# Kernel optimization log

Measured on AMD Instinct MI355X. Metric: run time of the kernel, lower is better.

## Reference

```python
import jax, jax.numpy as jnp
import numpy as np


def setup_inputs() -> dict:
    key = jax.random.key(0)
    ks = jax.random.split(key, 8)
    B, C, H, W = 4, 256, 64, 64
    s = 1.0 / np.sqrt(C)
    return {
        "x": jax.random.normal(ks[0], (B, C, H, W), jnp.float32),
        "y": jax.random.normal(ks[1], (B, C, H, W), jnp.float32),
        "Wq": jax.random.normal(ks[2], (C, C), jnp.float32) * s,
        "bq": jax.random.normal(ks[3], (C,), jnp.float32) * 0.01,
        "Wk": jax.random.normal(ks[4], (C, C), jnp.float32) * s,
        "bk": jax.random.normal(ks[5], (C,), jnp.float32) * 0.01,
        "Wv": jax.random.normal(ks[6], (C, C), jnp.float32) * s,
        "bv": jax.random.normal(ks[7], (C,), jnp.float32) * 0.01,
    }


def reference(x, y, Wq, bq, Wk, bk, Wv, bv):
    B, C, H, W = x.shape
    N = H * W
    # 1x1 convs == per-pixel linear over channels. Flatten spatial to N.
    xf = x.reshape(B, C, N)  # [B,C,N]
    yf = y.reshape(B, C, N)
    # q: [B,N,C]; k: [B,C,N]; v: [B,N,C]
    q = jnp.einsum('oc,bcn->bno', Wq, xf) + bq[None, None, :]
    k = jnp.einsum('oc,bcn->bon', Wk, yf) + bk[None, :, None]
    v = jnp.einsum('oc,bcn->bno', Wv, yf) + bv[None, None, :]
    # attention scores [B,N,N]; NOTE: original has no 1/sqrt(d) scaling.
    attn = jax.nn.softmax(jnp.einsum('bnc,bcm->bnm', q, k), axis=-1)
    out = jnp.einsum('bnm,bmc->bnc', attn, v)  # [B,N,C]
    return out.transpose(0, 2, 1).reshape(B, C, H, W)
```

## Files before the change

kernel.cpp:

```cpp
#include <hip/hip_runtime.h>


typedef __attribute__((ext_vector_type(8))) short short8;
typedef __attribute__((ext_vector_type(4))) float f32x4;
typedef __attribute__((ext_vector_type(4))) int int4v;
typedef __attribute__((ext_vector_type(8))) _Float16 half8;

#define LOG2E 1.44269504089f

static __device__ __forceinline__ float exp2_fast(float x){ return __builtin_amdgcn_exp2f(x); }

static __device__ __forceinline__ int pk_f16(float a, float b){
  auto h = __builtin_amdgcn_cvt_pkrtz(a, b);
  return __builtin_bit_cast(int, h);
}
static __device__ __forceinline__ unsigned short f2h(float v){
  return __builtin_bit_cast(unsigned short, (_Float16)v);
}

#define GLOAD16(gp, lp) __builtin_amdgcn_global_load_lds( \
  (const __attribute__((address_space(1))) void*)(gp),    \
  (__attribute__((address_space(3))) void*)(lp), 16, 0, 0)

#define MFMAF16(a,b,c) __builtin_amdgcn_mfma_f32_16x16x32_f16( \
  __builtin_bit_cast(half8, a), __builtin_bit_cast(half8, b), c, 0, 0, 0)

__global__ __launch_bounds__(256) void cvt_w(
    const float* __restrict__ wq, const float* __restrict__ wk,
    const float* __restrict__ wv, unsigned short* __restrict__ wf)
{
  const int o = blockIdx.x, t = blockIdx.y, c = threadIdx.x;
  const float* w = (t == 0) ? wq : ((t == 1) ? wk : wv);
  wf[t*65536 + o*256 + c] = f2h(w[o*256 + c]);
}

__global__ __launch_bounds__(256, 2) void proj_kernel(
    const float* __restrict__ x, const float* __restrict__ y,
    const unsigned short* __restrict__ wf,
    const float* __restrict__ bq, const float* __restrict__ bk, const float* __restrict__ bv,
    unsigned short* __restrict__ qf, unsigned short* __restrict__ kf,
    unsigned short* __restrict__ vtf)
{
  __shared__ float xs[256*64];
  __shared__ short wlds[2][4096];

  const int t   = blockIdx.z;
  const int b   = blockIdx.y;
  const int n0  = blockIdx.x * 64;
  const int tid = threadIdx.x;
  const int w   = tid >> 6, lane = tid & 63, g = lane >> 4, l15 = lane & 15;

  const float* src = ((t == 0) ? x : y) + (size_t)b*1048576 + n0;
  const char*  wt_b = (const char*)(wf + t*65536);

  int wsrc[2];
  #pragma unroll
  for (int i = 0; i < 2; i++){
    int s = w*2 + i;
    int row = s*2 + (lane >> 5);
    wsrc[i] = row*512 + (((lane & 31)*16) ^ ((row & 7) << 4));
  }

  #pragma unroll
  for (int i = 0; i < 16; i++){
    int c  = i*16 + (tid >> 4);
    int gg = (c >> 3) & 3;
    int sg = ((tid & 15) - 4*gg) & 15;
    GLOAD16((const char*)src + (size_t)c*16384 + sg*16,
            (char*)xs + (i*256 + tid)*16);
  }
  #pragma unroll
  for (int i = 0; i < 2; i++){
    int s = w*2 + i;
    GLOAD16(wt_b + wsrc[i], (char*)&wlds[0][0] + s*1024);
  }
  __syncthreads();

  int4v xf[8];
  {
    const int nn = (w*16 + l15 + 16*g) & 63;
    #pragma unroll
    for (int cs = 0; cs < 8; cs++){
      float v[8];
      #pragma unroll
      for (int j = 0; j < 8; j++) v[j] = xs[(cs*32 + g*8 + j)*64 + nn];
      int4v f;
      f[0] = pk_f16(v[0], v[1]); f[1] = pk_f16(v[2], v[3]);
      f[2] = pk_f16(v[4], v[5]); f[3] = pk_f16(v[6], v[7]);
      xf[cs] = f;
    }
  }

  const float* bias = (t == 0) ? bq : ((t == 1) ? bk : bv);

  int buf = 0;
  for (int ot = 0; ot < 16; ot++){
    if (ot < 15){
      #pragma unroll
      for (int i = 0; i < 2; i++){
        int s = w*2 + i;
        GLOAD16(wt_b + (ot+1)*8192 + wsrc[i], (char*)&wlds[buf^1][0] + s*1024);
      }
    }

    f32x4 acc;
    if (t < 2){
      float bo = bias[ot*16 + l15];
      acc = (f32x4){bo, bo, bo, bo};
    } else {
      acc = *(const f32x4*)&bias[ot*16 + g*4];
    }
    const char* wb = (const char*)&wlds[buf][0];
    #pragma unroll
    for (int cs = 0; cs < 8; cs++){
      short8 wfr = *(const short8*)(wb + (l15*512 + ((cs*64 + g*16) ^ ((l15 & 7) << 4))));
      if (t < 2) acc = MFMAF16(__builtin_bit_cast(short8, xf[cs]), wfr, acc);
      else       acc = MFMAF16(wfr, __builtin_bit_cast(short8, xf[cs]), acc);
    }
    if (t < 2){
      unsigned short* outp = (t == 0) ? qf : kf;
      #pragma unroll
      for (int r = 0; r < 4; r++){
        int n = n0 + w*16 + g*4 + r;
        outp[((size_t)(b*4096 + n))*256 + ot*16 + l15] = f2h(acc[r]);
      }
    } else {
      #pragma unroll
      for (int r = 0; r < 4; r++){
        int o = ot*16 + g*4 + r;
        vtf[((size_t)(b*256 + o))*4096 + n0 + w*16 + l15] = f2h(acc[r]);
      }
    }
    __syncthreads();
    buf ^= 1;
  }
}

__global__ __launch_bounds__(512, 2) void attn_kernel(
    const unsigned short* __restrict__ qf, const unsigned short* __restrict__ kf,
    const unsigned short* __restrict__ vtf,
    float* __restrict__ outp, unsigned short* __restrict__ part,
    float* __restrict__ mlbuf, int nsplit, int iters)
{
  __shared__ short k_s[3*32*256];
  __shared__ short v_s[3*256*32];

  const int tid  = threadIdx.x;
  const int w    = tid >> 6, lane = tid & 63, g = lane >> 4, col = lane & 15;
  const int bid  = blockIdx.x;

  int b, kvq, qt;
  if (nsplit == 4){
    int xcd = bid & 7, s = bid >> 3;
    int combo = xcd*2 + (s >> 4);
    qt = s & 15;  b = combo >> 2;  kvq = combo & 3;
  } else {
    int combo = bid & 7;
    qt = bid >> 3;  b = combo >> 1;  kvq = combo & 1;
  }
  const int qbase = qt * 256;

  short8 qh[2][8];
  #pragma unroll
  for (int nn = 0; nn < 2; nn++){
    const size_t qoff = ((size_t)(b*4096 + qbase + w*32 + nn*16 + col))*256 + g*8;
    #pragma unroll
    for (int ch = 0; ch < 8; ch++)
      qh[nn][ch] = *(const short8*)(qf + qoff + ch*32);
  }

  f32x4 o_acc[2][16];
  #pragma unroll
  for (int nn = 0; nn < 2; nn++)
    #pragma unroll
    for (int i = 0; i < 16; i++){
      o_acc[nn][i][0]=0.f; o_acc[nn][i][1]=0.f; o_acc[nn][i][2]=0.f; o_acc[nn][i][3]=0.f;
    }
  float mst[2] = {-1e30f, -1e30f};
  float lst[2] = {0.f, 0.f};

  const int swzK = (col & 7) << 4;
  const int g16  = g << 4;
  const int kb0  = col * 512;
  const int kb1  = kb0 + 8192;
  const int vb   = col*64 + (g16 ^ (((col>>1)&3)<<4));

  const int laneA  = col + ((g & 1) ? 32 : 0);
  const int laneB  = laneA + 16;
  const bool selLow = (g < 2);

  int ksrc[2], vsrc[2];
  #pragma unroll
  for (int i = 0; i < 2; i++){
    int s = w*2 + i;
    int m = s*2 + (lane >> 5);
    ksrc[i] = m*512 + (((lane & 31)*16) ^ ((m & 7) << 4));
    int c = s*16 + (lane >> 2);
    vsrc[i] = c*8192 + (((lane & 3)*16) ^ (((lane >> 3) & 3) << 4));
  }

  const int rows = 4096 / nsplit;
  const char* khg = (const char*)(kf + ((size_t)b*4096 + kvq*rows)*256);
  const char* vg  = (const char*)(vtf + ((size_t)b*256)*4096) + kvq*rows*2;

  #pragma unroll
  for (int i = 0; i < 2; i++){
    int s = w*2 + i;
    GLOAD16(khg + ksrc[i], (char*)k_s + s*1024);
    GLOAD16(vg  + vsrc[i], (char*)v_s + s*1024);
  }

  int cur = 0, nxt = 1;
  for (int it = 0; it < iters; ++it){
    if (it + 1 < iters){
      const char* kht = khg + (size_t)(it+1)*16384;
      const char* vtt = vg  + (size_t)(it+1)*64;
      const int ko = nxt*16384, vo = nxt*16384;
      #pragma unroll
      for (int i = 0; i < 2; i++){
        int s = w*2 + i;
        GLOAD16(kht + ksrc[i], (char*)k_s + ko + s*1024);
        GLOAD16(vtt + vsrc[i], (char*)v_s + vo + s*1024);
      }
      asm volatile("s_waitcnt vmcnt(4)" ::: "memory");
    } else {
      asm volatile("s_waitcnt vmcnt(0)" ::: "memory");
    }
    __builtin_amdgcn_s_barrier();
    __builtin_amdgcn_sched_barrier(0);

    const char* kb   = (const char*)k_s + cur*16384;
    const char* vbuf = (const char*)v_s + cur*16384;

    f32x4 s00 = {0.f,0.f,0.f,0.f}, s01 = {0.f,0.f,0.f,0.f};
    f32x4 s10 = {0.f,0.f,0.f,0.f}, s11 = {0.f,0.f,0.f,0.f};
    __builtin_amdgcn_s_setprio(1);
    #pragma unroll
    for (int ch = 0; ch < 8; ch++){
      int inr = ((ch << 6) | g16) ^ swzK;
      short8 kh0 = *(const short8*)(kb + kb0 + inr);
      short8 kh1 = *(const short8*)(kb + kb1 + inr);
      s00 = MFMAF16(kh0, qh[0][ch], s00);
      s01 = MFMAF16(kh1, qh[0][ch], s01);
      s10 = MFMAF16(kh0, qh[1][ch], s10);
      s11 = MFMAF16(kh1, qh[1][ch], s11);
    }
    __builtin_amdgcn_s_setprio(0);

    short8 pf[2];
    #pragma unroll
    for (int nn = 0; nn < 2; nn++){
      f32x4 s0 = nn ? s10 : s00;
      f32x4 s1 = nn ? s11 : s01;
      float tmax = fmaxf(fmaxf(fmaxf(s0[0],s0[1]), fmaxf(s0[2],s0[3])),
                         fmaxf(fmaxf(s1[0],s1[1]), fmaxf(s1[2],s1[3])));
      tmax = fmaxf(tmax, __shfl_xor(tmax, 16));
      tmax = fmaxf(tmax, __shfl_xor(tmax, 32));

      if (__any(tmax > mst[nn])){
        float mn = fmaxf(mst[nn], tmax);
        float sc = exp2_fast((mst[nn] - mn) * LOG2E);
        lst[nn] *= sc;
        #pragma unroll
        for (int i = 0; i < 16; i++){
          o_acc[nn][i][0]*=sc; o_acc[nn][i][1]*=sc;
          o_acc[nn][i][2]*=sc; o_acc[nn][i][3]*=sc;
        }
        mst[nn] = mn;
      }
      const float mb = mst[nn] * LOG2E;
      float p0 = exp2_fast(s0[0]*LOG2E - mb);
      float p1 = exp2_fast(s0[1]*LOG2E - mb);
      float p2 = exp2_fast(s0[2]*LOG2E - mb);
      float p3 = exp2_fast(s0[3]*LOG2E - mb);
      float p4 = exp2_fast(s1[0]*LOG2E - mb);
      float p5 = exp2_fast(s1[1]*LOG2E - mb);
      float p6 = exp2_fast(s1[2]*LOG2E - mb);
      float p7 = exp2_fast(s1[3]*LOG2E - mb);

      float psum = ((p0+p1)+(p2+p3)) + ((p4+p5)+(p6+p7));
      psum += __shfl_xor(psum, 16);
      psum += __shfl_xor(psum, 32);
      lst[nn] += psum;

      int W0 = pk_f16(p0, p1);
      int W1 = pk_f16(p2, p3);
      int W2 = pk_f16(p4, p5);
      int W3 = pk_f16(p6, p7);

      int a0 = __shfl(W0, laneA), a1 = __shfl(W1, laneA);
      int a2 = __shfl(W2, laneA), a3 = __shfl(W3, laneA);
      int b0 = __shfl(W0, laneB), b1 = __shfl(W1, laneB);
      int b2 = __shfl(W2, laneB), b3 = __shfl(W3, laneB);
      int4v ti;
      ti[0] = selLow ? a0 : a2;
      ti[1] = selLow ? a1 : a3;
      ti[2] = selLow ? b0 : b2;
      ti[3] = selLow ? b1 : b3;
      pf[nn] = __builtin_bit_cast(short8, ti);
    }

    __builtin_amdgcn_s_setprio(1);
    #pragma unroll
    for (int ct = 0; ct < 16; ct++){
      short8 vf = *(const short8*)(vbuf + ct*1024 + vb);
      o_acc[0][ct] = MFMAF16(vf, pf[0], o_acc[0][ct]);
      o_acc[1][ct] = MFMAF16(vf, pf[1], o_acc[1][ct]);
    }
    __builtin_amdgcn_s_setprio(0);

    cur = nxt;
    nxt = (nxt + 1 == 3) ? 0 : nxt + 1;
  }

  #pragma unroll
  for (int nn = 0; nn < 2; nn++){
    const int n = qbase + w*32 + nn*16 + col;
    if (kvq == 0){
      #pragma unroll
      for (int ct = 0; ct < 16; ct++)
        #pragma unroll
        for (int r = 0; r < 4; r++){
          int c = ct*16 + g*4 + r;
          outp[((size_t)(b*256 + c))*4096 + n] = o_acc[nn][ct][r];
        }
    } else {
      const size_t pbase = ((size_t)((kvq-1)*1024 + b*256))*4096;
      #pragma unroll
      for (int ct = 0; ct < 16; ct++)
        #pragma unroll
        for (int r = 0; r < 4; r++){
          int c = ct*16 + g*4 + r;
          part[pbase + (size_t)c*4096 + n] = f2h(o_acc[nn][ct][r]);
        }
    }
    if (g == 0){
      const size_t mb2 = ((size_t)(kvq*4 + b)*4096 + n)*2;
      mlbuf[mb2]     = mst[nn];
      mlbuf[mb2 + 1] = lst[nn];
    }
  }
}

__global__ __launch_bounds__(256) void merge_kernel(
    const unsigned short* __restrict__ part, const float* __restrict__ mlbuf,
    float* __restrict__ out, int nsplit)
{
  const int T    = blockIdx.x*256 + threadIdx.x;
  const int rowc = T >> 9;
  const int n8   = (T & 511) * 8;
  const int b    = rowc >> 8;

  float num[8], den[8], m[8];
  {
    f32x4 a0 = *(const f32x4*)&out[(size_t)rowc*4096 + n8];
    f32x4 a1 = *(const f32x4*)&out[(size_t)rowc*4096 + n8 + 4];
    const float* mlp = &mlbuf[((size_t)b*4096 + n8)*2];
    #pragma unroll
    for (int j = 0; j < 8; j++){
      m[j]   = mlp[j*2];
      den[j] = mlp[j*2 + 1];
      num[j] = (j < 4) ? a0[j] : a1[j-4];
    }
  }
  for (int s = 1; s < nsplit; s++){
    short8 pv = *(const short8*)&part[((size_t)((s-1)*1024 + rowc))*4096 + n8];
    const float* mlp = &mlbuf[((size_t)(s*4 + b)*4096 + n8)*2];
    #pragma unroll
    for (int j = 0; j < 8; j++){
      float ms = mlp[j*2], ls = mlp[j*2 + 1];
      unsigned short u = (unsigned short)pv[j];
      float ps = (float)*(const _Float16*)&u;
      float mn = fmaxf(m[j], ms);
      float sa = exp2_fast((m[j] - mn) * LOG2E);
      float sb = exp2_fast((ms   - mn) * LOG2E);
      num[j] = num[j]*sa + ps*sb;
      den[j] = den[j]*sa + ls*sb;
      m[j] = mn;
    }
  }
  f32x4 o0, o1;
  #pragma unroll
  for (int j = 0; j < 8; j++){
    float v = num[j] / den[j];
    if (j < 4) o0[j] = v; else o1[j-4] = v;
  }
  float* op = out + (size_t)rowc*4096 + n8;
  *(f32x4*)op       = o0;
  *(f32x4*)(op + 4) = o1;
}

extern "C" void kernel_launch(void* const* d_in, const int* in_sizes, int n_in,
                              void* d_out, int out_size, void* d_ws, size_t ws_size,
                              hipStream_t stream)
{
  const float* x  = (const float*)d_in[0];
  const float* y  = (const float*)d_in[1];
  const float* Wq = (const float*)d_in[2];
  const float* bq = (const float*)d_in[3];
  const float* Wk = (const float*)d_in[4];
  const float* bk = (const float*)d_in[5];
  const float* Wv = (const float*)d_in[6];
  const float* bv = (const float*)d_in[7];
  float* out = (float*)d_out;

  char* ws = (char*)d_ws;
  const size_t MB = 1048576;
  unsigned short* qf   = (unsigned short*)(ws + 0*MB);
  unsigned short* kfp  = (unsigned short*)(ws + 8*MB);
  unsigned short* vtf  = (unsigned short*)(ws + 16*MB);
  unsigned short* wf   = (unsigned short*)(ws + 24*MB);
  unsigned short* part = (unsigned short*)(ws + 24*MB + 393216);

  const int nsplit = (ws_size >= 50*MB) ? 4 : 2;
  const int iters  = (4096 / nsplit) / 32;
  float* mlb = (float*)(ws + 24*MB + 393216 + (size_t)(nsplit-1)*8*MB);

  cvt_w<<<dim3(256,3), dim3(256), 0, stream>>>(Wq, Wk, Wv, wf);
  proj_kernel<<<dim3(64,4,3), dim3(256), 0, stream>>>(x, y, wf, bq, bk, bv,
                                                      qf, kfp, vtf);
  attn_kernel<<<dim3(64*nsplit), dim3(512), 0, stream>>>(qf, kfp, vtf, out, part,
                                                         mlb, nsplit, iters);
  merge_kernel<<<dim3(2048), dim3(256), 0, stream>>>(part, mlb, out, nsplit);
}
```

Before: 159.7 us.

## Software-pipeline QK^T one tile ahead with 4-stage LDS ring buffer

Restructures the attention loop so the QK^T MFMAs for tile it+1 are issued before the softmax and PV work of tile it. K/V prefetch now runs two tiles ahead using a 4-deep LDS ring instead of a 3-deep one. The aim is to overlap matrix-core work with the exp/shuffle softmax phase and hide more global-load latency. The cost is more LDS (256KB of staging per 2 blocks may limit occupancy or fail launch_bounds(512,2)) and more live accumulator registers.

```diff
diff --git a/kernel.cpp b/kernel.cpp
--- a/kernel.cpp
+++ b/kernel.cpp
@@ -142,8 +142,8 @@
     float* __restrict__ outp, unsigned short* __restrict__ part,
     float* __restrict__ mlbuf, int nsplit, int iters)
 {
-  __shared__ short k_s[3*32*256];
-  __shared__ short v_s[3*256*32];
+  __shared__ short k_s[4*32*256];
+  __shared__ short v_s[4*256*32];
 
   const int tid  = threadIdx.x;
   const int w    = tid >> 6, lane = tid & 63, g = lane >> 4, col = lane & 15;
@@ -203,55 +203,79 @@
   const char* khg = (const char*)(kf + ((size_t)b*4096 + kvq*rows)*256);
   const char* vg  = (const char*)(vtf + ((size_t)b*256)*4096) + kvq*rows*2;
 
-  #pragma unroll
-  for (int i = 0; i < 2; i++){
-    int s = w*2 + i;
-    GLOAD16(khg + ksrc[i], (char*)k_s + s*1024);
-    GLOAD16(vg  + vsrc[i], (char*)v_s + s*1024);
-  }
-
-  int cur = 0, nxt = 1;
-  for (int it = 0; it < iters; ++it){
-    if (it + 1 < iters){
-      const char* kht = khg + (size_t)(it+1)*16384;
-      const char* vtt = vg  + (size_t)(it+1)*64;
-      const int ko = nxt*16384, vo = nxt*16384;
-      #pragma unroll
-      for (int i = 0; i < 2; i++){
-        int s = w*2 + i;
-        GLOAD16(kht + ksrc[i], (char*)k_s + ko + s*1024);
-        GLOAD16(vtt + vsrc[i], (char*)v_s + vo + s*1024);
-      }
-      asm volatile("s_waitcnt vmcnt(4)" ::: "memory");
-    } else {
-      asm volatile("s_waitcnt vmcnt(0)" ::: "memory");
-    }
-    __builtin_amdgcn_s_barrier();
-    __builtin_amdgcn_sched_barrier(0);
-
-    const char* kb   = (const char*)k_s + cur*16384;
-    const char* vbuf = (const char*)v_s + cur*16384;
-
-    f32x4 s00 = {0.f,0.f,0.f,0.f}, s01 = {0.f,0.f,0.f,0.f};
-    f32x4 s10 = {0.f,0.f,0.f,0.f}, s11 = {0.f,0.f,0.f,0.f};
+#define STAGE_TILE(T, BSEL) do {                                   \
+    const char* kht_ = khg + (size_t)(T)*16384;                    \
+    const char* vtt_ = vg  + (size_t)(T)*64;                       \
+    const int off_ = (BSEL)*16384;                                 \
+    _Pragma("unroll")                                              \
+    for (int i_ = 0; i_ < 2; i_++){                                \
+      int s_ = w*2 + i_;                                           \
+      GLOAD16(kht_ + ksrc[i_], (char*)k_s + off_ + s_*1024);       \
+      GLOAD16(vtt_ + vsrc[i_], (char*)v_s + off_ + s_*1024);       \
+    }                                                              \
+  } while (0)
+
+  STAGE_TILE(0, 0);
+  STAGE_TILE(1, 1);
+  asm volatile("s_waitcnt vmcnt(4)" ::: "memory");
+  __builtin_amdgcn_s_barrier();
+  __builtin_amdgcn_sched_barrier(0);
+
+  f32x4 n00 = {0.f,0.f,0.f,0.f}, n01 = {0.f,0.f,0.f,0.f};
+  f32x4 n10 = {0.f,0.f,0.f,0.f}, n11 = {0.f,0.f,0.f,0.f};
+  {
+    const char* kb = (const char*)k_s;
     __builtin_amdgcn_s_setprio(1);
     #pragma unroll
     for (int ch = 0; ch < 8; ch++){
       int inr = ((ch << 6) | g16) ^ swzK;
       short8 kh0 = *(const short8*)(kb + kb0 + inr);
       short8 kh1 = *(const short8*)(kb + kb1 + inr);
-      s00 = MFMAF16(kh0, qh[0][ch], s00);
-      s01 = MFMAF16(kh1, qh[0][ch], s01);
-      s10 = MFMAF16(kh0, qh[1][ch], s10);
-      s11 = MFMAF16(kh1, qh[1][ch], s11);
+      n00 = MFMAF16(kh0, qh[0][ch], n00);
+      n01 = MFMAF16(kh1, qh[0][ch], n01);
+      n10 = MFMAF16(kh0, qh[1][ch], n10);
+      n11 = MFMAF16(kh1, qh[1][ch], n11);
     }
     __builtin_amdgcn_s_setprio(0);
+  }
+
+  for (int it = 0; it < iters; ++it){
+    if (it + 2 < iters){
+      STAGE_TILE(it + 2, (it + 2) & 3);
+      asm volatile("s_waitcnt vmcnt(4)" ::: "memory");
+    } else {
+      asm volatile("s_waitcnt vmcnt(0)" ::: "memory");
+    }
+    if (it + 1 < iters){
+      __builtin_amdgcn_s_barrier();
+      __builtin_amdgcn_sched_barrier(0);
+    }
+
+    f32x4 c00 = n00, c01 = n01, c10 = n10, c11 = n11;
+
+    if (it + 1 < iters){
+      const char* kb = (const char*)k_s + ((it + 1) & 3)*16384;
+      n00 = (f32x4){0.f,0.f,0.f,0.f}; n01 = (f32x4){0.f,0.f,0.f,0.f};
+      n10 = (f32x4){0.f,0.f,0.f,0.f}; n11 = (f32x4){0.f,0.f,0.f,0.f};
+      __builtin_amdgcn_s_setprio(1);
+      #pragma unroll
+      for (int ch = 0; ch < 8; ch++){
+        int inr = ((ch << 6) | g16) ^ swzK;
+        short8 kh0 = *(const short8*)(kb + kb0 + inr);
+        short8 kh1 = *(const short8*)(kb + kb1 + inr);
+        n00 = MFMAF16(kh0, qh[0][ch], n00);
+        n01 = MFMAF16(kh1, qh[0][ch], n01);
+        n10 = MFMAF16(kh0, qh[1][ch], n10);
+        n11 = MFMAF16(kh1, qh[1][ch], n11);
+      }
+      __builtin_amdgcn_s_setprio(0);
+    }
 
     short8 pf[2];
     #pragma unroll
     for (int nn = 0; nn < 2; nn++){
-      f32x4 s0 = nn ? s10 : s00;
-      f32x4 s1 = nn ? s11 : s01;
+      f32x4 s0 = nn ? c10 : c00;
+      f32x4 s1 = nn ? c11 : c01;
       float tmax = fmaxf(fmaxf(fmaxf(s0[0],s0[1]), fmaxf(s0[2],s0[3])),
                          fmaxf(fmaxf(s1[0],s1[1]), fmaxf(s1[2],s1[3])));
       tmax = fmaxf(tmax, __shfl_xor(tmax, 16));
@@ -300,6 +324,7 @@
       pf[nn] = __builtin_bit_cast(short8, ti);
     }
 
+    const char* vbuf = (const char*)v_s + (it & 3)*16384;
     __builtin_amdgcn_s_setprio(1);
     #pragma unroll
     for (int ct = 0; ct < 16; ct++){
@@ -308,10 +333,8 @@
       o_acc[1][ct] = MFMAF16(vf, pf[1], o_acc[1][ct]);
     }
     __builtin_amdgcn_s_setprio(0);
-
-    cur = nxt;
-    nxt = (nxt + 1 == 3) ? 0 : nxt + 1;
-  }
+  }
+#undef STAGE_TILE
 
   #pragma unroll
   for (int nn = 0; nn < 2; nn++){
```

Result: slower. 180.6 us (+13.0%).

## Halve attention block size, double-buffer KV, add lazy rescale and normalized partials

Applied to the files above, without the earlier changes.

Shrinks attention blocks from 512 to 256 threads with 128 query rows each and doubles the grid, changing the XCD-aware block mapping to match. It replaces the triple-buffered async K/V staging with double buffering behind a full __syncthreads each iteration. The online-softmax rescale now runs only when the running max grows by more than 8, and partial outputs are normalized by l before storing to fp16, with the merge adjusted to match. The aim is more resident blocks and fewer rescale passes. In exchange, K/V overlap is shallower, each staged tile is reused across fewer queries, and the stale max allows exponent values up to e^8 in fp16 P.

```diff
diff --git a/kernel.cpp b/kernel.cpp
--- a/kernel.cpp
+++ b/kernel.cpp
@@ -136,14 +136,14 @@
   }
 }
 
-__global__ __launch_bounds__(512, 2) void attn_kernel(
+__global__ __launch_bounds__(256, 2) void attn_kernel(
     const unsigned short* __restrict__ qf, const unsigned short* __restrict__ kf,
     const unsigned short* __restrict__ vtf,
     float* __restrict__ outp, unsigned short* __restrict__ part,
     float* __restrict__ mlbuf, int nsplit, int iters)
 {
-  __shared__ short k_s[3*32*256];
-  __shared__ short v_s[3*256*32];
+  __shared__ short k_s[2*32*256];
+  __shared__ short v_s[2*256*32];
 
   const int tid  = threadIdx.x;
   const int w    = tid >> 6, lane = tid & 63, g = lane >> 4, col = lane & 15;
@@ -152,13 +152,13 @@
   int b, kvq, qt;
   if (nsplit == 4){
     int xcd = bid & 7, s = bid >> 3;
-    int combo = xcd*2 + (s >> 4);
-    qt = s & 15;  b = combo >> 2;  kvq = combo & 3;
+    int combo = xcd*2 + (s >> 5);
+    qt = s & 31;  b = combo >> 2;  kvq = combo & 3;
   } else {
     int combo = bid & 7;
     qt = bid >> 3;  b = combo >> 1;  kvq = combo & 1;
   }
-  const int qbase = qt * 256;
+  const int qbase = qt * 128;
 
   short8 qh[2][8];
   #pragma unroll
@@ -189,10 +189,10 @@
   const int laneB  = laneA + 16;
   const bool selLow = (g < 2);
 
-  int ksrc[2], vsrc[2];
-  #pragma unroll
-  for (int i = 0; i < 2; i++){
-    int s = w*2 + i;
+  int ksrc[4], vsrc[4];
+  #pragma unroll
+  for (int i = 0; i < 4; i++){
+    int s = w*4 + i;
     int m = s*2 + (lane >> 5);
     ksrc[i] = m*512 + (((lane & 31)*16) ^ ((m & 7) << 4));
     int c = s*16 + (lane >> 2);
@@ -203,34 +203,28 @@
   const char* khg = (const char*)(kf + ((size_t)b*4096 + kvq*rows)*256);
   const char* vg  = (const char*)(vtf + ((size_t)b*256)*4096) + kvq*rows*2;
 
-  #pragma unroll
-  for (int i = 0; i < 2; i++){
-    int s = w*2 + i;
-    GLOAD16(khg + ksrc[i], (char*)k_s + s*1024);
-    GLOAD16(vg  + vsrc[i], (char*)v_s + s*1024);
-  }
-
-  int cur = 0, nxt = 1;
+#define STAGE_TILE(T, BSEL) do {                                   \
+    const char* kht_ = khg + (size_t)(T)*16384;                    \
+    const char* vtt_ = vg  + (size_t)(T)*64;                       \
+    const int off_ = (BSEL)*16384;                                 \
+    _Pragma("unroll")                                              \
+    for (int i_ = 0; i_ < 4; i_++){                                \
+      int s_ = w*4 + i_;                                           \
+      GLOAD16(kht_ + ksrc[i_], (char*)k_s + off_ + s_*1024);       \
+      GLOAD16(vtt_ + vsrc[i_], (char*)v_s + off_ + s_*1024);       \
+    }                                                              \
+  } while (0)
+
+  STAGE_TILE(0, 0);
+
   for (int it = 0; it < iters; ++it){
-    if (it + 1 < iters){
-      const char* kht = khg + (size_t)(it+1)*16384;
-      const char* vtt = vg  + (size_t)(it+1)*64;
-      const int ko = nxt*16384, vo = nxt*16384;
-      #pragma unroll
-      for (int i = 0; i < 2; i++){
-        int s = w*2 + i;
-        GLOAD16(kht + ksrc[i], (char*)k_s + ko + s*1024);
-        GLOAD16(vtt + vsrc[i], (char*)v_s + vo + s*1024);
-      }
-      asm volatile("s_waitcnt vmcnt(4)" ::: "memory");
-    } else {
-      asm volatile("s_waitcnt vmcnt(0)" ::: "memory");
-    }
-    __builtin_amdgcn_s_barrier();
-    __builtin_amdgcn_sched_barrier(0);
-
-    const char* kb   = (const char*)k_s + cur*16384;
-    const char* vbuf = (const char*)v_s + cur*16384;
+    __syncthreads();
+
+    if (it + 1 < iters)
+      STAGE_TILE(it + 1, (it + 1) & 1);
+
+    const char* kb   = (const char*)k_s + (it & 1)*16384;
+    const char* vbuf = (const char*)v_s + (it & 1)*16384;
 
     f32x4 s00 = {0.f,0.f,0.f,0.f}, s01 = {0.f,0.f,0.f,0.f};
     f32x4 s10 = {0.f,0.f,0.f,0.f}, s11 = {0.f,0.f,0.f,0.f};
@@ -257,7 +251,7 @@
       tmax = fmaxf(tmax, __shfl_xor(tmax, 16));
       tmax = fmaxf(tmax, __shfl_xor(tmax, 32));
 
-      if (__any(tmax > mst[nn])){
+      if (__any(tmax > mst[nn] + 8.f)){
         float mn = fmaxf(mst[nn], tmax);
         float sc = exp2_fast((mst[nn] - mn) * LOG2E);
         lst[nn] *= sc;
@@ -308,21 +302,20 @@
       o_acc[1][ct] = MFMAF16(vf, pf[1], o_acc[1][ct]);
     }
     __builtin_amdgcn_s_setprio(0);
-
-    cur = nxt;
-    nxt = (nxt + 1 == 3) ? 0 : nxt + 1;
-  }
+  }
+#undef STAGE_TILE
 
   #pragma unroll
   for (int nn = 0; nn < 2; nn++){
     const int n = qbase + w*32 + nn*16 + col;
+    const float rl = 1.0f / lst[nn];
     if (kvq == 0){
       #pragma unroll
       for (int ct = 0; ct < 16; ct++)
         #pragma unroll
         for (int r = 0; r < 4; r++){
           int c = ct*16 + g*4 + r;
-          outp[((size_t)(b*256 + c))*4096 + n] = o_acc[nn][ct][r];
+          outp[((size_t)(b*256 + c))*4096 + n] = o_acc[nn][ct][r] * rl;
         }
     } else {
       const size_t pbase = ((size_t)((kvq-1)*1024 + b*256))*4096;
@@ -331,7 +324,7 @@
         #pragma unroll
         for (int r = 0; r < 4; r++){
           int c = ct*16 + g*4 + r;
-          part[pbase + (size_t)c*4096 + n] = f2h(o_acc[nn][ct][r]);
+          part[pbase + (size_t)c*4096 + n] = f2h(o_acc[nn][ct][r] * rl);
         }
     }
     if (g == 0){
@@ -360,7 +353,7 @@
     for (int j = 0; j < 8; j++){
       m[j]   = mlp[j*2];
       den[j] = mlp[j*2 + 1];
-      num[j] = (j < 4) ? a0[j] : a1[j-4];
+      num[j] = ((j < 4) ? a0[j] : a1[j-4]) * den[j];
     }
   }
   for (int s = 1; s < nsplit; s++){
@@ -374,7 +367,7 @@
       float mn = fmaxf(m[j], ms);
       float sa = exp2_fast((m[j] - mn) * LOG2E);
       float sb = exp2_fast((ms   - mn) * LOG2E);
-      num[j] = num[j]*sa + ps*sb;
+      num[j] = num[j]*sa + ps*ls*sb;
       den[j] = den[j]*sa + ls*sb;
       m[j] = mn;
     }
@@ -419,7 +412,7 @@
   cvt_w<<<dim3(256,3), dim3(256), 0, stream>>>(Wq, Wk, Wv, wf);
   proj_kernel<<<dim3(64,4,3), dim3(256), 0, stream>>>(x, y, wf, bq, bk, bv,
                                                       qf, kfp, vtf);
-  attn_kernel<<<dim3(64*nsplit), dim3(512), 0, stream>>>(qf, kfp, vtf, out, part,
-                                                         mlb, nsplit, iters);
+  attn_kernel<<<dim3(128*nsplit), dim3(256), 0, stream>>>(qf, kfp, vtf, out, part,
+                                                          mlb, nsplit, iters);
   merge_kernel<<<dim3(2048), dim3(256), 0, stream>>>(part, mlb, out, nsplit);
 }
```

New measurement: 175.0 us. 9.5% more time.
